# Kernel optimization log

Measured on AMD Instinct MI355X. Metric: run time of the kernel, lower is better.

## Reference

```python
import jax, jax.numpy as jnp
import numpy as np

H, E, V, MAXLEN, PAD = 8, 256, 1024, 64, 0


def _ln(x, g, b, eps):
    m = jnp.mean(x, -1, keepdims=True)
    v = jnp.mean((x - m) ** 2, -1, keepdims=True)
    return (x - m) / jnp.sqrt(v + eps) * g + b


def _get_pos(max_len, emb_dim):
    # replicates SVTISDPA.get_pos (sinusoidal, freq built via cumprod)
    half = emb_dim // 2
    freq = jnp.full((half,), 10000.0 ** (-1.0 / half), dtype=jnp.float32).at[0].set(1.0)
    freq = jnp.cumprod(freq)
    phase = jnp.arange(max_len, dtype=jnp.float32)[:, None] * freq[None, :]
    pe = jnp.zeros((max_len, emb_dim), dtype=jnp.float32)
    pe = pe.at[:, 0::2].set(jnp.sin(phase)).at[:, 1::2].set(jnp.cos(phase))
    return pe


def setup_inputs() -> dict:
    key = jax.random.key(0)
    ks = jax.random.split(key, 4)
    char_code = jax.random.randint(ks[0], (512, 64), 0, V)  # [B, max_len]
    emb_w = (jax.random.normal(ks[1], (V, E), dtype=jnp.float32) * 0.05).at[PAD].set(0.0)
    qkv_w = jax.random.normal(ks[2], (3 * E * H, E), dtype=jnp.float32) * 0.05
    fc_w = jax.random.normal(ks[3], (E, E * H), dtype=jnp.float32) * 0.05
    return {
        'char_code': char_code,
        'emb_w': emb_w,
        'qkv_w': qkv_w,
        'fc_w': fc_w,
        'fc_b': jnp.zeros((E,), jnp.float32),
        'sdpa_ln_g': jnp.ones((E,), jnp.float32),
        'sdpa_ln_b': jnp.zeros((E,), jnp.float32),
        'ff_ln_g': jnp.ones((E,), jnp.float32),
        'ff_ln_b': jnp.zeros((E,), jnp.float32),
        'bn_g': jnp.ones((E,), jnp.float32),
        'bn_b': jnp.zeros((E,), jnp.float32),
        'max_len': 64,
    }


def reference(char_code, emb_w, qkv_w, fc_w, fc_b, sdpa_ln_g, sdpa_ln_b,
              ff_ln_g, ff_ln_b, bn_g, bn_b, max_len):
    temp = E ** 0.5
    pos = _get_pos(MAXLEN, E)

    def qkv(x):
        y = (x @ qkv_w.T).reshape(x.shape[0], H, 3 * E)
        return y[..., :E], y[..., E:2 * E], y[..., 2 * E:]

    cq, ck, cv = qkv(emb_w)   # each [V, H, E]
    pq, pk, pv = qkv(pos)     # each [L, H, E]

    char_qk = jnp.einsum('vhe,whe->hvw', cq, ck) / temp          # [H,V,V]
    char_qk = char_qk.at[:, :, PAD].set(-1e9)
    pos_qk = jnp.einsum('lhe,mhe->hlm', pq, pk) / temp           # [H,L,L]
    char_pos_qk = (jnp.einsum('vhe,lhe->hvl', cq, pk)
                   + jnp.einsum('lhe,vhe->hvl', pq, ck)) / temp  # [H,V,L]

    c = char_code[:, :max_len]  # [B,M]
    M = max_len
    # sim[b,h,i,j] = char_qk[h,c_bi,c_bj] + char_pos_qk[h,c_bi,j] + pos_qk[h,i,j]
    sim = (char_qk[:, c[:, :, None], c[:, None, :]]
           + char_pos_qk[:, c, :M]).transpose(1, 0, 2, 3) \
          + pos_qk[None, :, :M, :M]                              # [B,H,M,M]
    attn = jax.nn.softmax(sim, axis=-1)

    not_mask = (c != PAD).astype(sim.dtype)                      # [B,M]
    n_words = jnp.sum(not_mask, -1)                              # [B]
    pooled = jnp.einsum('bm,bhmj->bhj', not_mask, attn) / n_words[:, None, None]

    v = cv[c].transpose(0, 2, 1, 3) + pv.transpose(1, 0, 2)[None, :, :M]  # [B,H,M,E]
    out = jnp.einsum('bhm,bhme->bhe', pooled, v).reshape(c.shape[0], H * E)
    out = _ln(out @ fc_w.T + fc_b, sdpa_ln_g, sdpa_ln_b, 1e-5)
    # FeedForward.forward returns layer_norm(x) (residual branch is dead code)
    out = _ln(out, ff_ln_g, ff_ln_b, 1e-6) + out
    return _ln(out, bn_g, bn_b, 1e-5)
```

## Files before the change

### kernel.cpp

```cpp
#include <hip/hip_runtime.h>
#include <math.h>

typedef unsigned short u16;
typedef __attribute__((ext_vector_type(4))) float f32x4;
typedef __attribute__((ext_vector_type(8))) short s16x8;
typedef __attribute__((ext_vector_type(4))) unsigned short u16x4;
typedef __attribute__((ext_vector_type(8))) unsigned short u16x8;

__device__ __forceinline__ u16 f2b(float f) {
  union { float f; unsigned u; } v; v.f = f;
  return (u16)((v.u + 0x7fffu + ((v.u >> 16) & 1u)) >> 16);
}
__device__ __forceinline__ float b2f(u16 b) {
  union { unsigned u; float f; } v; v.u = ((unsigned)b) << 16;
  return v.f;
}

__global__ void pos_kernel(u16* __restrict__ pe) {
  const int m = blockIdx.x;
  const int k = threadIdx.x;
  double f = pow(10000.0, -(double)k / 128.0);
  float ph = (float)m * (float)f;
  pe[m * 256 + 2 * k]     = f2b(sinf(ph));
  pe[m * 256 + 2 * k + 1] = f2b(cosf(ph));
}

__global__ __launch_bounds__(256) void gemm128(
    const float* __restrict__ embf, const u16* __restrict__ pe,
    const float* __restrict__ qkvf, const float* __restrict__ fcf,
    u16* __restrict__ Ccq, u16* __restrict__ Cpq, u16* __restrict__ fcx)
{
  const int ytile = blockIdx.y;
  const int tid = threadIdx.x;
  if (ytile == 9) {
    for (int q = blockIdx.x * 256 + tid; q < 131072; q += 48 * 256) {
      const int off4 = q * 4;
      const int row = off4 >> 11, col = off4 & 2047;
      f32x4 v = *(const f32x4*)&fcf[(size_t)off4];
      u16x4 o = { f2b(v[0]), f2b(v[1]), f2b(v[2]), f2b(v[3]) };
      *(u16x4*)&fcx[(size_t)row * 2560 + col] = o;
    }
    return;
  }
  __shared__ __align__(16) u16 As[128 * 64];
  __shared__ __align__(16) u16 Bs[128 * 64];
  u16* C; int m0;
  const bool peA = (ytile == 8);
  if (peA) { C = Cpq; m0 = 0; }
  else     { C = Ccq; m0 = ytile * 128; }
  const int n0 = blockIdx.x * 128;
  const int w = tid >> 6, l = tid & 63, hi = l >> 4, lo = l & 15;
  const int wr = (w >> 1) * 64, wc = (w & 1) * 64;
  const int srow = tid >> 3, scol = (tid & 7) * 8;
  f32x4 acc[4][4] = {};
  for (int k0 = 0; k0 < 256; k0 += 64) {
    __syncthreads();
    #pragma unroll
    for (int q = 0; q < 4; ++q) {
      const int row = q * 32 + srow;
      const int sidx = row * 64 + (scol ^ ((row & 7) << 3));
      if (peA) {
        *(u16x8*)&As[sidx] = *(const u16x8*)&pe[(long)row * 256 + k0 + scol];
      } else {
        f32x4 a0 = *(const f32x4*)&embf[(long)(m0 + row) * 256 + k0 + scol];
        f32x4 a1 = *(const f32x4*)&embf[(long)(m0 + row) * 256 + k0 + scol + 4];
        u16x8 oa = { f2b(a0[0]), f2b(a0[1]), f2b(a0[2]), f2b(a0[3]),
                     f2b(a1[0]), f2b(a1[1]), f2b(a1[2]), f2b(a1[3]) };
        *(u16x8*)&As[sidx] = oa;
      }
      f32x4 b0 = *(const f32x4*)&qkvf[(long)(n0 + row) * 256 + k0 + scol];
      f32x4 b1 = *(const f32x4*)&qkvf[(long)(n0 + row) * 256 + k0 + scol + 4];
      u16x8 ob = { f2b(b0[0]), f2b(b0[1]), f2b(b0[2]), f2b(b0[3]),
                   f2b(b1[0]), f2b(b1[1]), f2b(b1[2]), f2b(b1[3]) };
      *(u16x8*)&Bs[sidx] = ob;
    }
    __syncthreads();
    #pragma unroll
    for (int kk = 0; kk < 2; ++kk) {
      s16x8 a[4], bf[4];
      #pragma unroll
      for (int m = 0; m < 4; ++m) {
        const int ar = wr + m * 16 + lo;
        a[m] = *(const s16x8*)&As[ar * 64 + ((hi * 8 + kk * 32) ^ ((ar & 7) << 3))];
      }
      #pragma unroll
      for (int n = 0; n < 4; ++n) {
        const int br = wc + n * 16 + lo;
        bf[n] = *(const s16x8*)&Bs[br * 64 + ((hi * 8 + kk * 32) ^ ((br & 7) << 3))];
      }
      #pragma unroll
      for (int m = 0; m < 4; ++m)
        #pragma unroll
        for (int n = 0; n < 4; ++n)
          acc[m][n] = __builtin_amdgcn_mfma_f32_16x16x32_bf16(a[m], bf[n], acc[m][n], 0, 0, 0);
    }
  }
  #pragma unroll
  for (int m = 0; m < 4; ++m)
    #pragma unroll
    for (int n = 0; n < 4; ++n)
      #pragma unroll
      for (int r = 0; r < 4; ++r)
        C[(long)(m0 + wr + m * 16 + hi * 4 + r) * 6144 + n0 + wc + n * 16 + lo] = f2b(acc[m][n][r]);
}

__global__ __launch_bounds__(256) void gemm_bf(
    const u16* __restrict__ A, int lda, long sA,
    const u16* __restrict__ B, int ldb, long sB,
    float* __restrict__ C, int ldc, long sC, int K)
{
  __shared__ __align__(16) u16 As[64 * 64];
  __shared__ __align__(16) u16 Bs[64 * 64];
  const int z = blockIdx.z;
  A += (long)z * sA;  B += (long)z * sB;
  const int m0 = blockIdx.y * 64, n0 = blockIdx.x * 64;
  const int tid = threadIdx.x;
  const int r8 = tid >> 3, s8t = (tid & 7) * 8;
  const int w = tid >> 6, l = tid & 63, hi = l >> 4, lo = l & 15;
  f32x4 acc[4] = {};
  for (int k0 = 0; k0 < K; k0 += 64) {
    __syncthreads();
    #pragma unroll
    for (int q = 0; q < 2; ++q) {
      const int row = q * 32 + r8;
      const int sidx = row * 64 + (s8t ^ ((row & 7) << 3));
      *(u16x8*)&As[sidx] = *(const u16x8*)&A[(long)(m0 + row) * lda + k0 + s8t];
      *(u16x8*)&Bs[sidx] = *(const u16x8*)&B[(long)(n0 + row) * ldb + k0 + s8t];
    }
    __syncthreads();
    #pragma unroll
    for (int kk = 0; kk < 2; ++kk) {
      const int arow = w * 16 + lo;
      s16x8 a = *(const s16x8*)&As[arow * 64 + ((hi * 8 + kk * 32) ^ ((arow & 7) << 3))];
      #pragma unroll
      for (int n = 0; n < 4; ++n) {
        const int brow = n * 16 + lo;
        s16x8 bfr = *(const s16x8*)&Bs[brow * 64 + ((hi * 8 + kk * 32) ^ ((brow & 7) << 3))];
        acc[n] = __builtin_amdgcn_mfma_f32_16x16x32_bf16(a, bfr, acc[n], 0, 0, 0);
      }
    }
  }
  const long zoff = (long)z * sC;
  #pragma unroll
  for (int n = 0; n < 4; ++n)
    #pragma unroll
    for (int r = 0; r < 4; ++r)
      C[zoff + (long)(m0 + w * 16 + hi * 4 + r) * ldc + n0 + n * 16 + lo] = acc[n][r];
}

__global__ __launch_bounds__(256) void tables_kernel(
    const u16* __restrict__ cqkv, const u16* __restrict__ pqkv,
    const u16* __restrict__ fcx,
    u16* __restrict__ cpqk, u16* __restrict__ pqk, u16* __restrict__ pvfc)
{
  __shared__ __align__(16) u16 As1[64 * 64], Bs1[64 * 64];
  __shared__ __align__(16) u16 As2[64 * 64], Bs2[64 * 64];
  const int blk = blockIdx.x;
  const u16 *A1, *A2 = nullptr, *B1, *B2 = nullptr;
  u16* C; int lda, ldb, ldc, m0; bool dual = false;
  if (blk < 128) {
    const int h = blk & 7, mt = blk >> 3;
    A1 = cqkv + h * 768 + 256; A2 = cqkv + h * 768;
    B1 = pqkv + h * 768;       B2 = pqkv + h * 768 + 256;
    lda = 6144; ldb = 6144; C = cpqk + (long)h * 65536; ldc = 64;
    m0 = mt * 64; dual = true;
  } else if (blk < 136) {
    const int h = blk - 128;
    A1 = pqkv + h * 768; B1 = pqkv + h * 768 + 256;
    lda = 6144; ldb = 6144; C = pqk + h * 4096; ldc = 64; m0 = 0;
  } else {
    const int idx = blk - 136, h = idx & 7, mt = idx >> 3;
    A1 = fcx + h * 256; B1 = pqkv + 512 + h * 768;
    lda = 2560; ldb = 6144; C = pvfc + h * 64; ldc = 2560; m0 = mt * 64;
  }
  const int tid = threadIdx.x;
  const int r8 = tid >> 3, s8t = (tid & 7) * 8;
  const int w = tid >> 6, l = tid & 63, hi = l >> 4, lo = l & 15;
  f32x4 acc[4] = {};
  for (int k0 = 0; k0 < 256; k0 += 64) {
    __syncthreads();
    #pragma unroll
    for (int q = 0; q < 2; ++q) {
      const int row = q * 32 + r8;
      const int sidx = row * 64 + (s8t ^ ((row & 7) << 3));
      *(u16x8*)&As1[sidx] = *(const u16x8*)&A1[(long)(m0 + row) * lda + k0 + s8t];
      *(u16x8*)&Bs1[sidx] = *(const u16x8*)&B1[(long)row * ldb + k0 + s8t];
      if (dual) {
        *(u16x8*)&As2[sidx] = *(const u16x8*)&A2[(long)(m0 + row) * lda + k0 + s8t];
        *(u16x8*)&Bs2[sidx] = *(const u16x8*)&B2[(long)row * ldb + k0 + s8t];
      }
    }
    __syncthreads();
    #pragma unroll
    for (int kk = 0; kk < 2; ++kk) {
      const int arow = w * 16 + lo;
      const int aidx = arow * 64 + ((hi * 8 + kk * 32) ^ ((arow & 7) << 3));
      s16x8 a1 = *(const s16x8*)&As1[aidx];
      #pragma unroll
      for (int n = 0; n < 4; ++n) {
        const int brow = n * 16 + lo;
        const int bidx = brow * 64 + ((hi * 8 + kk * 32) ^ ((brow & 7) << 3));
        acc[n] = __builtin_amdgcn_mfma_f32_16x16x32_bf16(a1, *(const s16x8*)&Bs1[bidx], acc[n], 0, 0, 0);
      }
      if (dual) {
        s16x8 a2 = *(const s16x8*)&As2[aidx];
        #pragma unroll
        for (int n = 0; n < 4; ++n) {
          const int brow = n * 16 + lo;
          const int bidx = brow * 64 + ((hi * 8 + kk * 32) ^ ((brow & 7) << 3));
          acc[n] = __builtin_amdgcn_mfma_f32_16x16x32_bf16(a2, *(const s16x8*)&Bs2[bidx], acc[n], 0, 0, 0);
        }
      }
    }
  }
  #pragma unroll
  for (int n = 0; n < 4; ++n)
    #pragma unroll
    for (int r = 0; r < 4; ++r)
      C[(long)(m0 + w * 16 + hi * 4 + r) * ldc + n * 16 + lo] = f2b(acc[n][r]);
}

__global__ __launch_bounds__(256, 4) void attn_kernel(
    const int* __restrict__ cc, const u16* __restrict__ cqkv,
    const u16* __restrict__ cpqk, const u16* __restrict__ pqk,
    u16* __restrict__ outp)
{
  __shared__ __align__(16) u16 Ks[64 * 256];
  const int h = blockIdx.x, b = blockIdx.y;
  const int tid = threadIdx.x;
  const long hq = (long)h * 768;

  const int w = tid >> 6, l = tid & 63, hi = l >> 4, lo = l & 15;
  const int r8 = tid >> 3, s8t = (tid & 7) * 8;
  const int rb = r8 + 32;

  const int cl = cc[b * 64 + l];
  const float invn = 1.f / (float)__popcll(__ballot(cl != 0));

  const int ca = __shfl(cl, r8), cb2 = __shfl(cl, rb);
  const long rowa = (long)ca * 6144 + hq;
  const long rowb = (long)cb2 * 6144 + hq;

  u16x8 kr[8];
  #pragma unroll
  for (int p = 0; p < 4; ++p) {
    kr[p]     = *(const u16x8*)&cqkv[rowa + 256 + p * 64 + s8t];
    kr[p + 4] = *(const u16x8*)&cqkv[rowb + 256 + p * 64 + s8t];
  }
  u16x8 vr[8];
  #pragma unroll
  for (int p = 0; p < 4; ++p) {
    vr[p]     = *(const u16x8*)&cqkv[rowa + 512 + p * 64 + s8t];
    vr[p + 4] = *(const u16x8*)&cqkv[rowb + 512 + p * 64 + s8t];
  }
  u16x8 cta = *(const u16x8*)&cpqk[((long)h * 1024 + ca) * 64 + s8t];
  u16x8 ctb = *(const u16x8*)&cpqk[((long)h * 1024 + cb2) * 64 + s8t];
  u16x8 pta = *(const u16x8*)&pqk[(long)h * 4096 + (long)r8 * 64 + s8t];
  u16x8 ptb = *(const u16x8*)&pqk[(long)h * 4096 + (long)rb * 64 + s8t];
  const long qrow = (long)__shfl(cl, w * 16 + lo) * 6144 + hq;
  s16x8 a[8];
  #pragma unroll
  for (int kk = 0; kk < 8; ++kk)
    a[kk] = *(const s16x8*)&cqkv[qrow + kk * 32 + hi * 8];

  #pragma unroll
  for (int p = 0; p < 4; ++p) {
    *(u16x8*)&Ks[r8 * 256 + ((p * 64 + s8t) ^ ((r8 & 7) << 3))] = kr[p];
    *(u16x8*)&Ks[rb * 256 + ((p * 64 + s8t) ^ ((rb & 7) << 3))] = kr[p + 4];
  }
  __syncthreads();

  f32x4 acc[4] = {};
  #pragma unroll
  for (int kk = 0; kk < 8; ++kk) {
    #pragma unroll
    for (int n = 0; n < 4; ++n) {
      const int brow = n * 16 + lo;
      s16x8 bfr = *(const s16x8*)&Ks[brow * 256 + ((hi * 8 + kk * 32) ^ ((brow & 7) << 3))];
      acc[n] = __builtin_amdgcn_mfma_f32_16x16x32_bf16(a[kk], bfr, acc[n], 0, 0, 0);
    }
  }
  __syncthreads();

  {
    u16x8 t0, t1;
    #pragma unroll
    for (int d = 0; d < 8; ++d) {
      t0[d] = f2b(b2f(cta[d]) + b2f(pta[d]));
      t1[d] = f2b(b2f(ctb[d]) + b2f(ptb[d]));
    }
    *(u16x8*)&Ks[r8 * 64 + (s8t ^ ((r8 & 7) << 3))] = t0;
    *(u16x8*)&Ks[rb * 64 + (s8t ^ ((rb & 7) << 3))] = t1;
  }
  __syncthreads();

  const float scale = 0.0625f;
  int csj[4];
  #pragma unroll
  for (int n = 0; n < 4; ++n) csj[n] = __shfl(cl, n * 16 + lo);
  float ex[4][4];
  float wgt[4];
  #pragma unroll
  for (int r = 0; r < 4; ++r) {
    const int i = w * 16 + hi * 4 + r;
    const int tswz = (i & 7) << 3;
    float s[4];
    float mx = -3e38f;
    #pragma unroll
    for (int n = 0; n < 4; ++n) {
      const int j = n * 16 + lo;
      float v = (acc[n][r] + b2f(Ks[i * 64 + (j ^ tswz)])) * scale;
      if (csj[n] == 0) v = -1e9f;
      s[n] = v;
      mx = fmaxf(mx, v);
    }
    mx = fmaxf(mx, __shfl_xor(mx, 1));
    mx = fmaxf(mx, __shfl_xor(mx, 2));
    mx = fmaxf(mx, __shfl_xor(mx, 4));
    mx = fmaxf(mx, __shfl_xor(mx, 8));
    float sum = 0.f;
    #pragma unroll
    for (int n = 0; n < 4; ++n) { const float e = __expf(s[n] - mx); ex[n][r] = e; sum += e; }
    sum += __shfl_xor(sum, 1);
    sum += __shfl_xor(sum, 2);
    sum += __shfl_xor(sum, 4);
    sum += __shfl_xor(sum, 8);
    wgt[r] = (__shfl(cl, i) != 0 ? 1.f : 0.f) / sum;
  }
  float* poolpF = (float*)&Ks[8192];
  #pragma unroll
  for (int n = 0; n < 4; ++n) {
    float cp = ex[n][0] * wgt[0] + ex[n][1] * wgt[1] + ex[n][2] * wgt[2] + ex[n][3] * wgt[3];
    cp += __shfl_xor(cp, 16);
    cp += __shfl_xor(cp, 32);
    if (hi == 0) poolpF[w * 64 + n * 16 + lo] = cp;
  }
  __syncthreads();

  const float pla = (poolpF[r8] + poolpF[64 + r8] + poolpF[128 + r8] + poolpF[192 + r8]) * invn;
  const float plb = (poolpF[rb] + poolpF[64 + rb] + poolpF[128 + rb] + poolpF[192 + rb]) * invn;
  if ((tid & 7) == 0) {
    outp[(long)b * 2560 + 2048 + h * 64 + r8] = f2b(pla);
    outp[(long)b * 2560 + 2048 + h * 64 + rb] = f2b(plb);
  }
  __syncthreads();

  #pragma unroll
  for (int p = 0; p < 4; ++p) {
    u16x8 t0, t1;
    #pragma unroll
    for (int d = 0; d < 8; ++d) {
      t0[d] = f2b(pla * b2f(vr[p][d]));
      t1[d] = f2b(plb * b2f(vr[p + 4][d]));
    }
    *(u16x8*)&Ks[r8 * 256 + ((p * 64 + s8t) ^ ((r8 & 7) << 3))] = t0;
    *(u16x8*)&Ks[rb * 256 + ((p * 64 + s8t) ^ ((rb & 7) << 3))] = t1;
  }
  __syncthreads();

  float o = 0.f;
  #pragma unroll
  for (int j = 0; j < 64; ++j)
    o += b2f(Ks[j * 256 + (tid ^ ((j & 7) << 3))]);
  outp[(long)b * 2560 + h * 256 + tid] = f2b(o);
}

__global__ __launch_bounds__(256) void ln_chain(
    const float* __restrict__ xp, const float* __restrict__ fcb,
    const float* __restrict__ g1, const float* __restrict__ b1,
    const float* __restrict__ g2, const float* __restrict__ b2,
    const float* __restrict__ g3, const float* __restrict__ b3,
    float* __restrict__ out)
{
  __shared__ float red[4];
  const int b = blockIdx.x, t = threadIdx.x;
  const long idx = (long)b * 256 + t;
  float v = fcb[t];
  #pragma unroll
  for (int z = 0; z < 8; ++z) v += xp[idx + (long)z * 131072];

  auto bsum = [&](float val) -> float {
    #pragma unroll
    for (int o = 32; o; o >>= 1) val += __shfl_down(val, o);
    __syncthreads();
    if ((t & 63) == 0) red[t >> 6] = val;
    __syncthreads();
    return red[0] + red[1] + red[2] + red[3];
  };

  float mean = bsum(v) * (1.f / 256.f);
  float d = v - mean;
  float var = bsum(d * d) * (1.f / 256.f);
  const float y1 = d * rsqrtf(var + 1e-5f) * g1[t] + b1[t];

  mean = bsum(y1) * (1.f / 256.f);
  d = y1 - mean;
  var = bsum(d * d) * (1.f / 256.f);
  const float y2 = d * rsqrtf(var + 1e-6f) * g2[t] + b2[t] + y1;

  mean = bsum(y2) * (1.f / 256.f);
  d = y2 - mean;
  var = bsum(d * d) * (1.f / 256.f);
  out[idx] = d * rsqrtf(var + 1e-5f) * g3[t] + b3[t];
}

extern "C" void kernel_launch(void* const* d_in, const int* in_sizes, int n_in,
                              void* d_out, int out_size, void* d_ws, size_t ws_size,
                              hipStream_t stream) {
  (void)in_sizes; (void)n_in; (void)out_size; (void)ws_size;
  const int*   cc    = (const int*)  d_in[0];
  const float* emb_w = (const float*)d_in[1];
  const float* qkv_w = (const float*)d_in[2];
  const float* fc_w  = (const float*)d_in[3];
  const float* fc_b  = (const float*)d_in[4];
  const float* sg    = (const float*)d_in[5];
  const float* sb    = (const float*)d_in[6];
  const float* fg    = (const float*)d_in[7];
  const float* fb    = (const float*)d_in[8];
  const float* bg    = (const float*)d_in[9];
  const float* bbv   = (const float*)d_in[10];
  float* out = (float*)d_out;

  char* p = (char*)d_ws;
  u16* pe_pad  = (u16*)p;  p += (size_t)128 * 256 * 2;
  u16* fcx     = (u16*)p;  p += (size_t)256 * 2560 * 2;
  u16* cqkv_bf = (u16*)p;  p += (size_t)1024 * 6144 * 2;
  u16* pqkv_bf = (u16*)p;  p += (size_t)128 * 6144 * 2;
  u16* cpqk16  = (u16*)p;  p += (size_t)8 * 1024 * 64 * 2;
  u16* pqk16   = (u16*)p;  p += (size_t)8 * 64 * 64 * 2;
  u16* sdpa_bf = (u16*)p;  p += (size_t)512 * 2560 * 2;
  float* fco   = (float*)p; p += (size_t)8 * 512 * 256 * 4;

  pos_kernel<<<dim3(64), dim3(128), 0, stream>>>(pe_pad);

  gemm128<<<dim3(48, 10), dim3(256), 0, stream>>>(
      emb_w, pe_pad, qkv_w, fc_w, cqkv_bf, pqkv_bf, fcx);

  tables_kernel<<<dim3(168), dim3(256), 0, stream>>>(
      cqkv_bf, pqkv_bf, fcx, cpqk16, pqk16, fcx + 2048);

  attn_kernel<<<dim3(8, 512), dim3(256), 0, stream>>>(
      cc, cqkv_bf, cpqk16, pqk16, sdpa_bf);

  gemm_bf<<<dim3(4, 8, 8), dim3(256), 0, stream>>>(
      sdpa_bf, 2560, 320, fcx, 2560, 320, fco, 256, (long)512 * 256, 320);

  ln_chain<<<dim3(512), dim3(256), 0, stream>>>(fco, fc_b, sg, sb, fg, fb, bg, bbv, out);
}
```

Before: 85.84 us.

## Fuse positional encoding into QKV GEMM and stage attention Q rows through LDS

Drops the separate pos_kernel launch and computes the sinusoidal positional encoding inline while loading the A tile of the QKV GEMM, using fast exp and sincos intrinsics. In the attention kernel, Q rows are now loaded coalesced into shared memory and read back as MFMA fragments, replacing scattered per-lane global loads. V loads are deferred until after the K store to lower register pressure. This costs an extra LDS round trip and barrier, and the fast-math sincos/exp may differ slightly from the previous double-precision pow, and from the reference's cumprod-built frequencies, in the last bits.

```diff
diff --git a/kernel.cpp b/kernel.cpp
--- a/kernel.cpp
+++ b/kernel.cpp
@@ -16,18 +16,9 @@
   return v.f;
 }
 
-__global__ void pos_kernel(u16* __restrict__ pe) {
-  const int m = blockIdx.x;
-  const int k = threadIdx.x;
-  double f = pow(10000.0, -(double)k / 128.0);
-  float ph = (float)m * (float)f;
-  pe[m * 256 + 2 * k]     = f2b(sinf(ph));
-  pe[m * 256 + 2 * k + 1] = f2b(cosf(ph));
-}
-
 __global__ __launch_bounds__(256) void gemm128(
-    const float* __restrict__ embf, const u16* __restrict__ pe,
-    const float* __restrict__ qkvf, const float* __restrict__ fcf,
+    const float* __restrict__ embf, const float* __restrict__ qkvf,
+    const float* __restrict__ fcf,
     u16* __restrict__ Ccq, u16* __restrict__ Cpq, u16* __restrict__ fcx)
 {
   const int ytile = blockIdx.y;
@@ -60,7 +51,20 @@
       const int row = q * 32 + srow;
       const int sidx = row * 64 + (scol ^ ((row & 7) << 3));
       if (peA) {
-        *(u16x8*)&As[sidx] = *(const u16x8*)&pe[(long)row * 256 + k0 + scol];
+        u16x8 oa = {0, 0, 0, 0, 0, 0, 0, 0};
+        if (row < 64) {
+          #pragma unroll
+          for (int d2 = 0; d2 < 4; ++d2) {
+            const int kf = ((k0 + scol) >> 1) + d2;
+            const float fr = __expf(-(float)kf * 0.07195578415606394f);
+            const float ph = (float)row * fr;
+            float s, c;
+            __sincosf(ph, &s, &c);
+            oa[d2 * 2]     = f2b(s);
+            oa[d2 * 2 + 1] = f2b(c);
+          }
+        }
+        *(u16x8*)&As[sidx] = oa;
       } else {
         f32x4 a0 = *(const f32x4*)&embf[(long)(m0 + row) * 256 + k0 + scol];
         f32x4 a1 = *(const f32x4*)&embf[(long)(m0 + row) * 256 + k0 + scol + 4];
@@ -233,6 +237,7 @@
   const int w = tid >> 6, l = tid & 63, hi = l >> 4, lo = l & 15;
   const int r8 = tid >> 3, s8t = (tid & 7) * 8;
   const int rb = r8 + 32;
+  const int swa = (r8 & 7) << 3, swb = (rb & 7) << 3;
 
   const int cl = cc[b * 64 + l];
   const float invn = 1.f / (float)__popcll(__ballot(cl != 0));
@@ -241,32 +246,48 @@
   const long rowa = (long)ca * 6144 + hq;
   const long rowb = (long)cb2 * 6144 + hq;
 
+  u16x8 qr[8];
+  #pragma unroll
+  for (int p = 0; p < 4; ++p) {
+    qr[p]     = *(const u16x8*)&cqkv[rowa + p * 64 + s8t];
+    qr[p + 4] = *(const u16x8*)&cqkv[rowb + p * 64 + s8t];
+  }
   u16x8 kr[8];
   #pragma unroll
   for (int p = 0; p < 4; ++p) {
     kr[p]     = *(const u16x8*)&cqkv[rowa + 256 + p * 64 + s8t];
     kr[p + 4] = *(const u16x8*)&cqkv[rowb + 256 + p * 64 + s8t];
-  }
-  u16x8 vr[8];
-  #pragma unroll
-  for (int p = 0; p < 4; ++p) {
-    vr[p]     = *(const u16x8*)&cqkv[rowa + 512 + p * 64 + s8t];
-    vr[p + 4] = *(const u16x8*)&cqkv[rowb + 512 + p * 64 + s8t];
   }
   u16x8 cta = *(const u16x8*)&cpqk[((long)h * 1024 + ca) * 64 + s8t];
   u16x8 ctb = *(const u16x8*)&cpqk[((long)h * 1024 + cb2) * 64 + s8t];
   u16x8 pta = *(const u16x8*)&pqk[(long)h * 4096 + (long)r8 * 64 + s8t];
   u16x8 ptb = *(const u16x8*)&pqk[(long)h * 4096 + (long)rb * 64 + s8t];
-  const long qrow = (long)__shfl(cl, w * 16 + lo) * 6144 + hq;
+
+  #pragma unroll
+  for (int p = 0; p < 4; ++p) {
+    *(u16x8*)&Ks[r8 * 256 + ((p * 64 + s8t) ^ swa)] = qr[p];
+    *(u16x8*)&Ks[rb * 256 + ((p * 64 + s8t) ^ swb)] = qr[p + 4];
+  }
+  __syncthreads();
+
+  const int arow = w * 16 + lo;
+  const int aswz = (arow & 7) << 3;
   s16x8 a[8];
   #pragma unroll
   for (int kk = 0; kk < 8; ++kk)
-    a[kk] = *(const s16x8*)&cqkv[qrow + kk * 32 + hi * 8];
-
-  #pragma unroll
-  for (int p = 0; p < 4; ++p) {
-    *(u16x8*)&Ks[r8 * 256 + ((p * 64 + s8t) ^ ((r8 & 7) << 3))] = kr[p];
-    *(u16x8*)&Ks[rb * 256 + ((p * 64 + s8t) ^ ((rb & 7) << 3))] = kr[p + 4];
+    a[kk] = *(const s16x8*)&Ks[arow * 256 + ((hi * 8 + kk * 32) ^ aswz)];
+  __syncthreads();
+
+  #pragma unroll
+  for (int p = 0; p < 4; ++p) {
+    *(u16x8*)&Ks[r8 * 256 + ((p * 64 + s8t) ^ swa)] = kr[p];
+    *(u16x8*)&Ks[rb * 256 + ((p * 64 + s8t) ^ swb)] = kr[p + 4];
+  }
+  u16x8 vr[8];
+  #pragma unroll
+  for (int p = 0; p < 4; ++p) {
+    vr[p]     = *(const u16x8*)&cqkv[rowa + 512 + p * 64 + s8t];
+    vr[p + 4] = *(const u16x8*)&cqkv[rowb + 512 + p * 64 + s8t];
   }
   __syncthreads();
 
@@ -289,8 +310,8 @@
       t0[d] = f2b(b2f(cta[d]) + b2f(pta[d]));
       t1[d] = f2b(b2f(ctb[d]) + b2f(ptb[d]));
     }
-    *(u16x8*)&Ks[r8 * 64 + (s8t ^ ((r8 & 7) << 3))] = t0;
-    *(u16x8*)&Ks[rb * 64 + (s8t ^ ((rb & 7) << 3))] = t1;
+    *(u16x8*)&Ks[r8 * 64 + (s8t ^ swa)] = t0;
+    *(u16x8*)&Ks[rb * 64 + (s8t ^ swb)] = t1;
   }
   __syncthreads();
 
@@ -353,8 +374,8 @@
       t0[d] = f2b(pla * b2f(vr[p][d]));
       t1[d] = f2b(plb * b2f(vr[p + 4][d]));
     }
-    *(u16x8*)&Ks[r8 * 256 + ((p * 64 + s8t) ^ ((r8 & 7) << 3))] = t0;
-    *(u16x8*)&Ks[rb * 256 + ((p * 64 + s8t) ^ ((rb & 7) << 3))] = t1;
+    *(u16x8*)&Ks[r8 * 256 + ((p * 64 + s8t) ^ swa)] = t0;
+    *(u16x8*)&Ks[rb * 256 + ((p * 64 + s8t) ^ swb)] = t1;
   }
   __syncthreads();
 
@@ -422,7 +443,6 @@
   float* out = (float*)d_out;
 
   char* p = (char*)d_ws;
-  u16* pe_pad  = (u16*)p;  p += (size_t)128 * 256 * 2;
   u16* fcx     = (u16*)p;  p += (size_t)256 * 2560 * 2;
   u16* cqkv_bf = (u16*)p;  p += (size_t)1024 * 6144 * 2;
   u16* pqkv_bf = (u16*)p;  p += (size_t)128 * 6144 * 2;
@@ -431,10 +451,8 @@
   u16* sdpa_bf = (u16*)p;  p += (size_t)512 * 2560 * 2;
   float* fco   = (float*)p; p += (size_t)8 * 512 * 256 * 4;
 
-  pos_kernel<<<dim3(64), dim3(128), 0, stream>>>(pe_pad);
-
   gemm128<<<dim3(48, 10), dim3(256), 0, stream>>>(
-      emb_w, pe_pad, qkv_w, fc_w, cqkv_bf, pqkv_bf, fcx);
+      emb_w, qkv_w, fc_w, cqkv_bf, pqkv_bf, fcx);
 
   tables_kernel<<<dim3(168), dim3(256), 0, stream>>>(
       cqkv_bf, pqkv_bf, fcx, cpqk16, pqk16, fcx + 2048);
```

After: 83.91 us. 1.02x faster.
